# Kernel tuning notes

Hardware: AMD Instinct MI355X
Metric: run time of the kernel (lower is better)

The kernel has to match this reference:

```python
import jax, jax.numpy as jnp
import numpy as np

N_NODES = 50000
N_EDGES = 800000
IN_DIM = 128
HID = 128
OUT_DIM = 128
N_LAYERS = 6
NUM_GRAPHS = 128


def setup_inputs() -> dict:
    key = jax.random.key(0)
    ks = jax.random.split(key, 16)
    s = 0.05
    inp = {
        "x": jax.random.normal(ks[0], (N_NODES, IN_DIM), jnp.float32),
        "edge_index": jax.random.randint(ks[1], (2, N_EDGES), 0, N_NODES, jnp.int64 if jax.config.jax_enable_x64 else jnp.int32).astype(jnp.int32),
        "batch": jnp.sort(jax.random.randint(ks[2], (N_NODES,), 0, NUM_GRAPHS).astype(jnp.int32)),
        # pre linear
        "pre_w": jax.random.normal(ks[3], (IN_DIM, HID), jnp.float32) * s,
        "pre_b": jnp.zeros((HID,), jnp.float32),
        # GIN mlp per layer: Linear(H,H) -> ReLU -> Linear(H,H)
        "conv_w1": jax.random.normal(ks[4], (N_LAYERS, HID, HID), jnp.float32) * s,
        "conv_b1": jnp.zeros((N_LAYERS, HID), jnp.float32),
        "conv_w2": jax.random.normal(ks[5], (N_LAYERS, HID, HID), jnp.float32) * s,
        "conv_b2": jnp.zeros((N_LAYERS, HID), jnp.float32),
        # post MLP: Linear(7H, H) -> ReLU -> Linear(H, out)
        "post_w1": jax.random.normal(ks[6], (HID * (N_LAYERS + 1), HID), jnp.float32) * s,
        "post_b1": jnp.zeros((HID,), jnp.float32),
        "post_w2": jax.random.normal(ks[7], (HID, OUT_DIM), jnp.float32) * s,
        "post_b2": jnp.zeros((OUT_DIM,), jnp.float32),
    }
    return inp


def reference(x, edge_index, batch, pre_w, pre_b, conv_w1, conv_b1, conv_w2, conv_b2,
              post_w1, post_b1, post_w2, post_b2):
    src, dst = edge_index[0], edge_index[1]
    # pre linear
    h = x @ pre_w + pre_b  # [N, H]
    emb_list = [h]
    xres = h
    for i in range(N_LAYERS):
        # GINConv (eps=0): agg_j x_j over in-edges, then (1+eps)*x + agg -> MLP
        msg = h[src]  # [E, H] gather
        agg = jax.ops.segment_sum(msg, dst, num_segments=N_NODES)  # scatter-add
        z = h + agg
        z = jax.nn.relu(z @ conv_w1[i] + conv_b1[i]) @ conv_w2[i] + conv_b2[i]
        if i & 1:
            z = z + xres
            xres = z
        h = jax.nn.relu(z)
        emb_list.append(h)
    emb = jnp.concatenate(emb_list, axis=1)  # [N, (L+1)*H]
    # global add pool over graphs
    pooled = jax.ops.segment_sum(emb, batch, num_segments=NUM_GRAPHS)  # [G, (L+1)*H]
    out = jax.nn.relu(pooled @ post_w1 + post_b1) @ post_w2 + post_b2  # [G, OUT]
    return out
```

## Files before the change

kernel.cpp:

```cpp
#include <hip/hip_runtime.h>
#include <hip/hip_bf16.h>

#define HID 128

using bf16x8 = __attribute__((ext_vector_type(8))) short;
using f32x4  = __attribute__((ext_vector_type(4))) float;

__device__ inline float bf2f(unsigned int u16) {
    union { float f; unsigned int i; } v; v.i = u16 << 16; return v.f;
}
__device__ inline unsigned short f2bf(float f) {
    __hip_bfloat16 h = __float2bfloat16(f);
    return *reinterpret_cast<unsigned short*>(&h);
}


__global__ void zero_i32(int* __restrict__ p, int n) {
    int i = blockIdx.x * blockDim.x + threadIdx.x;
    if (i < n) p[i] = 0;
}

__global__ void count_deg(const int* __restrict__ dst, int* __restrict__ deg, int E) {
    int e = blockIdx.x * blockDim.x + threadIdx.x;
    if (e < E) atomicAdd(&deg[dst[e]], 1);
}

__global__ __launch_bounds__(256) void block_sums(const int* __restrict__ deg,
                                                  int* __restrict__ bsum, int n) {
    __shared__ int red[256];
    int t = threadIdx.x;
    int i = blockIdx.x * 256 + t;
    red[t] = (i < n) ? deg[i] : 0;
    __syncthreads();
    for (int off = 128; off > 0; off >>= 1) {
        if (t < off) red[t] += red[t + off];
        __syncthreads();
    }
    if (t == 0) bsum[blockIdx.x] = red[0];
}

__global__ __launch_bounds__(1024) void scan_bsums(const int* __restrict__ bsum,
                                                   int* __restrict__ bstart, int nb) {
    __shared__ int s[1024];
    int t = threadIdx.x;
    s[t] = (t < nb) ? bsum[t] : 0;
    __syncthreads();
    for (int off = 1; off < 1024; off <<= 1) {
        int v = (t >= off) ? s[t - off] : 0;
        __syncthreads();
        s[t] += v;
        __syncthreads();
    }
    if (t < nb) bstart[t] = (t == 0) ? 0 : s[t - 1];
}

__global__ __launch_bounds__(256) void scan_within(const int* __restrict__ deg,
                                                   const int* __restrict__ bstart,
                                                   int* __restrict__ row_ptr,
                                                   int* __restrict__ pos, int n) {
    __shared__ int s[256];
    int b = blockIdx.x, t = threadIdx.x;
    int i = b * 256 + t;
    int v = (i < n) ? deg[i] : 0;
    s[t] = v;
    __syncthreads();
    for (int off = 1; off < 256; off <<= 1) {
        int u = (t >= off) ? s[t - off] : 0;
        __syncthreads();
        s[t] += u;
        __syncthreads();
    }
    if (i < n) {
        int excl = bstart[b] + s[t] - v;
        row_ptr[i] = excl;
        pos[i] = excl;
        if (i == n - 1) row_ptr[n] = bstart[b] + s[t];
    }
}

__global__ void fill_csr(const int* __restrict__ src, const int* __restrict__ dst,
                         int* __restrict__ pos, int* __restrict__ csr_src, int E) {
    int e = blockIdx.x * blockDim.x + threadIdx.x;
    if (e < E) {
        int p = atomicAdd(&pos[dst[e]], 1);
        csr_src[p] = src[e];
    }
}

__global__ void graph_starts(const int* __restrict__ batch, int* __restrict__ gstart,
                             int n, int G) {
    int g = blockIdx.x * blockDim.x + threadIdx.x;
    if (g > G) return;
    int lo = 0, hi = n;
    while (lo < hi) { int m = (lo + hi) >> 1; if (batch[m] < g) lo = m + 1; else hi = m; }
    gstart[g] = lo;
}


__global__ void f32_to_bf16_vec(const float* __restrict__ in,
                                unsigned short* __restrict__ out, int n8) {
    int i = blockIdx.x * blockDim.x + threadIdx.x;
    if (i >= n8) return;
    const float4* in4 = (const float4*)in;
    float4 a = in4[i * 2], b = in4[i * 2 + 1];
    uint4 o;
    o.x = f2bf(a.x) | ((unsigned)f2bf(a.y) << 16);
    o.y = f2bf(a.z) | ((unsigned)f2bf(a.w) << 16);
    o.z = f2bf(b.x) | ((unsigned)f2bf(b.y) << 16);
    o.w = f2bf(b.z) | ((unsigned)f2bf(b.w) << 16);
    ((uint4*)out)[i] = o;
}

__global__ void transpose_kc(const float* __restrict__ W, unsigned short* __restrict__ Wt,
                             int K, int C, int total) {
    int tid = blockIdx.x * blockDim.x + threadIdx.x;
    if (tid >= total) return;
    int kc = K * C;
    int mat = tid / kc;
    int rem = tid - mat * kc;
    int c = rem / K;
    int k = rem - c * K;
    Wt[tid] = f2bf(W[(size_t)mat * kc + (size_t)k * C + c]);
}

__global__ __launch_bounds__(256) void agg_kernel(const unsigned short* __restrict__ emb,
                                                  int slice_u4, int row_u4,
                                                  const int* __restrict__ row_ptr,
                                                  const int* __restrict__ csr_src,
                                                  unsigned short* __restrict__ z, int N) {
    int node = blockIdx.x * 16 + (threadIdx.x >> 4);
    int lane = threadIdx.x & 15;
    if (node >= N) return;
    const uint4* h4 = (const uint4*)emb;
    uint4 u = h4[(size_t)node * row_u4 + slice_u4 + lane];
    float s0 = bf2f(u.x & 0xffff), s1 = bf2f(u.x >> 16);
    float s2 = bf2f(u.y & 0xffff), s3 = bf2f(u.y >> 16);
    float s4 = bf2f(u.z & 0xffff), s5 = bf2f(u.z >> 16);
    float s6 = bf2f(u.w & 0xffff), s7 = bf2f(u.w >> 16);
    int e0 = row_ptr[node], e1 = row_ptr[node + 1];
    int e = e0;
    for (; e + 3 < e1; e += 4) {
        int sa = csr_src[e], sb = csr_src[e + 1], sc = csr_src[e + 2], sd = csr_src[e + 3];
        uint4 va = h4[(size_t)sa * row_u4 + slice_u4 + lane];
        uint4 vb = h4[(size_t)sb * row_u4 + slice_u4 + lane];
        uint4 vc = h4[(size_t)sc * row_u4 + slice_u4 + lane];
        uint4 vd = h4[(size_t)sd * row_u4 + slice_u4 + lane];
        s0 += bf2f(va.x & 0xffff); s1 += bf2f(va.x >> 16);
        s2 += bf2f(va.y & 0xffff); s3 += bf2f(va.y >> 16);
        s4 += bf2f(va.z & 0xffff); s5 += bf2f(va.z >> 16);
        s6 += bf2f(va.w & 0xffff); s7 += bf2f(va.w >> 16);
        s0 += bf2f(vb.x & 0xffff); s1 += bf2f(vb.x >> 16);
        s2 += bf2f(vb.y & 0xffff); s3 += bf2f(vb.y >> 16);
        s4 += bf2f(vb.z & 0xffff); s5 += bf2f(vb.z >> 16);
        s6 += bf2f(vb.w & 0xffff); s7 += bf2f(vb.w >> 16);
        s0 += bf2f(vc.x & 0xffff); s1 += bf2f(vc.x >> 16);
        s2 += bf2f(vc.y & 0xffff); s3 += bf2f(vc.y >> 16);
        s4 += bf2f(vc.z & 0xffff); s5 += bf2f(vc.z >> 16);
        s6 += bf2f(vc.w & 0xffff); s7 += bf2f(vc.w >> 16);
        s0 += bf2f(vd.x & 0xffff); s1 += bf2f(vd.x >> 16);
        s2 += bf2f(vd.y & 0xffff); s3 += bf2f(vd.y >> 16);
        s4 += bf2f(vd.z & 0xffff); s5 += bf2f(vd.z >> 16);
        s6 += bf2f(vd.w & 0xffff); s7 += bf2f(vd.w >> 16);
    }
    for (; e < e1; e++) {
        uint4 va = h4[(size_t)csr_src[e] * row_u4 + slice_u4 + lane];
        s0 += bf2f(va.x & 0xffff); s1 += bf2f(va.x >> 16);
        s2 += bf2f(va.y & 0xffff); s3 += bf2f(va.y >> 16);
        s4 += bf2f(va.z & 0xffff); s5 += bf2f(va.z >> 16);
        s6 += bf2f(va.w & 0xffff); s7 += bf2f(va.w >> 16);
    }
    uint4 o;
    o.x = f2bf(s0) | ((unsigned)f2bf(s1) << 16);
    o.y = f2bf(s2) | ((unsigned)f2bf(s3) << 16);
    o.z = f2bf(s4) | ((unsigned)f2bf(s5) << 16);
    o.w = f2bf(s6) | ((unsigned)f2bf(s7) << 16);
    ((uint4*)z)[(size_t)node * 16 + lane] = o;
}

template <bool ODD>
__global__ __launch_bounds__(128) void fused_gemm12(const unsigned short* __restrict__ z,
                                                    const unsigned short* __restrict__ Wt1,
                                                    const float* __restrict__ b1,
                                                    const unsigned short* __restrict__ Wt2,
                                                    const float* __restrict__ b2,
                                                    unsigned short* __restrict__ xres,
                                                    unsigned short* __restrict__ h_out,
                                                    int out_stride, int N) {
    __shared__ __align__(16) char lds[16 * 256];
    int t = threadIdx.x;
    int wave = t >> 6, lane = t & 63, l15 = lane & 15, l4 = lane >> 4;
    int rowbase = blockIdx.x * 16;
    int colbase = wave * 64;

    f32x4 acc[4];
#pragma unroll
    for (int ct = 0; ct < 4; ct++) acc[ct] = (f32x4){0.f, 0.f, 0.f, 0.f};

    int r0 = min(rowbase + l15, N - 1);
#pragma unroll
    for (int kk = 0; kk < 4; kk++) {
        int k0 = kk * 32 + l4 * 8;
        bf16x8 a0 = *(const bf16x8*)&z[(size_t)r0 * HID + k0];
#pragma unroll
        for (int ct = 0; ct < 4; ct++) {
            bf16x8 b = *(const bf16x8*)&Wt1[(size_t)(colbase + ct * 16 + l15) * HID + k0];
            acc[ct] = __builtin_amdgcn_mfma_f32_16x16x32_bf16(a0, b, acc[ct], 0, 0, 0);
        }
    }

#pragma unroll
    for (int ct = 0; ct < 4; ct++) {
        int col = colbase + ct * 16 + l15;
        float bc = b1[col];
#pragma unroll
        for (int j = 0; j < 4; j++) {
            int r = l4 * 4 + j;
            float v = fmaxf(acc[ct][j] + bc, 0.f);
            *(unsigned short*)(lds + r * 256 + ((col * 2) ^ ((r & 7) << 4))) = f2bf(v);
        }
    }
    __syncthreads();

#pragma unroll
    for (int ct = 0; ct < 4; ct++) acc[ct] = (f32x4){0.f, 0.f, 0.f, 0.f};
#pragma unroll
    for (int kk = 0; kk < 4; kk++) {
        int k0 = kk * 32 + l4 * 8;
        bf16x8 a0 = *(const bf16x8*)(lds + l15 * 256 + ((k0 * 2) ^ ((l15 & 7) << 4)));
#pragma unroll
        for (int ct = 0; ct < 4; ct++) {
            bf16x8 b = *(const bf16x8*)&Wt2[(size_t)(colbase + ct * 16 + l15) * HID + k0];
            acc[ct] = __builtin_amdgcn_mfma_f32_16x16x32_bf16(a0, b, acc[ct], 0, 0, 0);
        }
    }

#pragma unroll
    for (int ct = 0; ct < 4; ct++) {
        int col = colbase + ct * 16 + l15;
        float bc = b2[col];
#pragma unroll
        for (int j = 0; j < 4; j++) {
            int r = l4 * 4 + j;
            int rg = rowbase + r;
            if (rg < N) {
                float v = acc[ct][j] + bc;
                if (ODD) {
                    v += bf2f(xres[(size_t)rg * HID + col]);
                    xres[(size_t)rg * HID + col] = f2bf(v);
                }
                h_out[(size_t)rg * out_stride + col] = f2bf(fmaxf(v, 0.f));
            }
        }
    }
}

__global__ __launch_bounds__(256) void linear_pre(const unsigned short* __restrict__ in,
                                                  const unsigned short* __restrict__ Wt,
                                                  const float* __restrict__ bias,
                                                  unsigned short* __restrict__ out,
                                                  int out_stride,
                                                  unsigned short* __restrict__ pre_out, int M) {
    int tid = threadIdx.x;
    int wave = tid >> 6, lane = tid & 63;
    int l15 = lane & 15, l4 = lane >> 4;
    int rowbase = blockIdx.x * 64 + wave * 16;
    f32x4 acc[8];
#pragma unroll
    for (int ct = 0; ct < 8; ct++) acc[ct] = (f32x4){0.f, 0.f, 0.f, 0.f};
    int r0 = min(rowbase + l15, M - 1);
#pragma unroll
    for (int kk = 0; kk < 4; kk++) {
        int k0 = kk * 32 + l4 * 8;
        bf16x8 a0 = *(const bf16x8*)&in[(size_t)r0 * HID + k0];
#pragma unroll
        for (int ct = 0; ct < 8; ct++) {
            bf16x8 b = *(const bf16x8*)&Wt[(size_t)(ct * 16 + l15) * HID + k0];
            acc[ct] = __builtin_amdgcn_mfma_f32_16x16x32_bf16(a0, b, acc[ct], 0, 0, 0);
        }
    }
#pragma unroll
    for (int ct = 0; ct < 8; ct++) {
        int col = ct * 16 + l15;
        float bc = bias[col];
#pragma unroll
        for (int j = 0; j < 4; j++) {
            int r = rowbase + l4 * 4 + j;
            if (r < M) {
                float v = acc[ct][j] + bc;
                unsigned short bv = f2bf(v);
                pre_out[(size_t)r * HID + col] = bv;
                out[(size_t)r * out_stride + col] = bv;
            }
        }
    }
}

__global__ __launch_bounds__(128) void pool_all(const unsigned short* __restrict__ emb,
                                                const int* __restrict__ gstart,
                                                float* __restrict__ part, int EMB) {
    int g = blockIdx.x >> 3, sub = blockIdx.x & 7;
    int t = threadIdx.x;
    if (t >= 112) return;
    const uint4* e4 = (const uint4*)emb;
    int row_u4 = EMB / 8;
    int n0 = gstart[g], n1 = gstart[g + 1];
    float s[8] = {0.f, 0.f, 0.f, 0.f, 0.f, 0.f, 0.f, 0.f};
    for (int n = n0 + sub; n < n1; n += 8) {
        uint4 v = e4[(size_t)n * row_u4 + t];
        s[0] += bf2f(v.x & 0xffff); s[1] += bf2f(v.x >> 16);
        s[2] += bf2f(v.y & 0xffff); s[3] += bf2f(v.y >> 16);
        s[4] += bf2f(v.z & 0xffff); s[5] += bf2f(v.z >> 16);
        s[6] += bf2f(v.w & 0xffff); s[7] += bf2f(v.w >> 16);
    }
    float4* p4 = (float4*)&part[(size_t)blockIdx.x * EMB + t * 8];
    p4[0] = (float4){s[0], s[1], s[2], s[3]};
    p4[1] = (float4){s[4], s[5], s[6], s[7]};
}

__global__ __launch_bounds__(128) void pool_fin(const float* __restrict__ part,
                                                unsigned short* __restrict__ pooled,
                                                int EMB) {
    int idx = blockIdx.x * 128 + threadIdx.x;
    int g = idx / EMB, c = idx - g * EMB;
    float s = 0.f;
#pragma unroll
    for (int sub = 0; sub < 8; sub++)
        s += part[(size_t)(g * 8 + sub) * EMB + c];
    pooled[idx] = f2bf(s);
}

__global__ __launch_bounds__(256) void post_mfma(const unsigned short* __restrict__ pooled,
                                                 const unsigned short* __restrict__ w1t,
                                                 const float* __restrict__ b1,
                                                 const unsigned short* __restrict__ w2t,
                                                 const float* __restrict__ b2,
                                                 float* __restrict__ out, int EMB) {
    __shared__ __align__(16) char lds[128 * 256];
    int t = threadIdx.x;
    int wave = t >> 6, lane = t & 63, l15 = lane & 15, l4 = lane >> 4;
    int wrow = wave * 32;
    f32x4 acc[2][8];
#pragma unroll
    for (int rt = 0; rt < 2; rt++)
#pragma unroll
        for (int ct = 0; ct < 8; ct++) acc[rt][ct] = (f32x4){0.f, 0.f, 0.f, 0.f};
    int r0 = wrow + l15, r1 = r0 + 16;
#pragma unroll 4
    for (int kk = 0; kk < EMB / 32; kk++) {
        int k0 = kk * 32 + l4 * 8;
        bf16x8 a0 = *(const bf16x8*)&pooled[(size_t)r0 * EMB + k0];
        bf16x8 a1 = *(const bf16x8*)&pooled[(size_t)r1 * EMB + k0];
#pragma unroll
        for (int ct = 0; ct < 8; ct++) {
            bf16x8 b = *(const bf16x8*)&w1t[(size_t)(ct * 16 + l15) * EMB + k0];
            acc[0][ct] = __builtin_amdgcn_mfma_f32_16x16x32_bf16(a0, b, acc[0][ct], 0, 0, 0);
            acc[1][ct] = __builtin_amdgcn_mfma_f32_16x16x32_bf16(a1, b, acc[1][ct], 0, 0, 0);
        }
    }
#pragma unroll
    for (int ct = 0; ct < 8; ct++) {
        int col = ct * 16 + l15;
        float bc = b1[col];
#pragma unroll
        for (int rt = 0; rt < 2; rt++)
#pragma unroll
            for (int j = 0; j < 4; j++) {
                int r = wrow + rt * 16 + l4 * 4 + j;
                float v = fmaxf(acc[rt][ct][j] + bc, 0.f);
                *(unsigned short*)(lds + r * 256 + ((col * 2) ^ ((r & 7) << 4))) = f2bf(v);
            }
    }
    __syncthreads();
#pragma unroll
    for (int rt = 0; rt < 2; rt++)
#pragma unroll
        for (int ct = 0; ct < 8; ct++) acc[rt][ct] = (f32x4){0.f, 0.f, 0.f, 0.f};
#pragma unroll
    for (int kk = 0; kk < 4; kk++) {
        int k0 = kk * 32 + l4 * 8;
        bf16x8 a0 = *(const bf16x8*)(lds + r0 * 256 + ((k0 * 2) ^ ((r0 & 7) << 4)));
        bf16x8 a1 = *(const bf16x8*)(lds + r1 * 256 + ((k0 * 2) ^ ((r1 & 7) << 4)));
#pragma unroll
        for (int ct = 0; ct < 8; ct++) {
            bf16x8 b = *(const bf16x8*)&w2t[(size_t)(ct * 16 + l15) * HID + k0];
            acc[0][ct] = __builtin_amdgcn_mfma_f32_16x16x32_bf16(a0, b, acc[0][ct], 0, 0, 0);
            acc[1][ct] = __builtin_amdgcn_mfma_f32_16x16x32_bf16(a1, b, acc[1][ct], 0, 0, 0);
        }
    }
#pragma unroll
    for (int ct = 0; ct < 8; ct++) {
        int col = ct * 16 + l15;
        float bc = b2[col];
#pragma unroll
        for (int rt = 0; rt < 2; rt++)
#pragma unroll
            for (int j = 0; j < 4; j++) {
                int r = wrow + rt * 16 + l4 * 4 + j;
                out[(size_t)r * HID + col] = acc[rt][ct][j] + bc;
            }
    }
}


extern "C" void kernel_launch(void* const* d_in, const int* in_sizes, int n_in,
                              void* d_out, int out_size, void* d_ws, size_t ws_size,
                              hipStream_t stream) {
    const float* x       = (const float*)d_in[0];
    const int* edge_index= (const int*)d_in[1];
    const int* batch     = (const int*)d_in[2];
    const float* pre_w   = (const float*)d_in[3];
    const float* pre_b   = (const float*)d_in[4];
    const float* conv_w1 = (const float*)d_in[5];
    const float* conv_b1 = (const float*)d_in[6];
    const float* conv_w2 = (const float*)d_in[7];
    const float* conv_b2 = (const float*)d_in[8];
    const float* post_w1 = (const float*)d_in[9];
    const float* post_b1 = (const float*)d_in[10];
    const float* post_w2 = (const float*)d_in[11];
    const float* post_b2 = (const float*)d_in[12];
    float* outp = (float*)d_out;

    int N = in_sizes[0] / HID;
    int E = in_sizes[1] / 2;
    int L = in_sizes[5] / (HID * HID);
    int G = out_size / HID;
    int EMB = (L + 1) * HID;

    const int* src = edge_index;
    const int* dst = edge_index + E;

    char* w = (char*)d_ws;
    auto alloc = [&](size_t bytes) -> char* {
        char* p = w;
        w += (bytes + 255) & ~(size_t)255;
        return p;
    };
    unsigned short* emb   = (unsigned short*)alloc((size_t)N * EMB * 2);
    unsigned short* z_bf  = (unsigned short*)alloc((size_t)N * HID * 2);
    unsigned short* xres  = (unsigned short*)alloc((size_t)N * HID * 2);
    float* part   = (float*)alloc((size_t)G * 8 * EMB * 4);
    unsigned short* pooled = (unsigned short*)alloc((size_t)G * EMB * 2);
    unsigned short* Wt_pre = (unsigned short*)alloc((size_t)HID * HID * 2);
    unsigned short* Wt_c1  = (unsigned short*)alloc((size_t)L * HID * HID * 2);
    unsigned short* Wt_c2  = (unsigned short*)alloc((size_t)L * HID * HID * 2);
    unsigned short* w1t    = (unsigned short*)alloc((size_t)EMB * HID * 2);
    unsigned short* w2t    = (unsigned short*)alloc((size_t)HID * HID * 2);
    int* deg      = (int*)alloc((size_t)(N + 1) * 4);
    int* row_ptr  = (int*)alloc((size_t)(N + 1) * 4);
    int* pos      = (int*)alloc((size_t)(N + 1) * 4);
    int* bsum     = (int*)alloc((size_t)1024 * 4);
    int* bstart   = (int*)alloc((size_t)1024 * 4);
    int* csr_src  = (int*)alloc((size_t)E * 4);
    int* gstart   = (int*)alloc((size_t)(G + 1) * 4);
    (void)ws_size; (void)n_in;

    int eb = (E + 255) / 256;
    int nb = (N + 255) / 256;

    zero_i32<<<nb, 256, 0, stream>>>(deg, N);
    count_deg<<<eb, 256, 0, stream>>>(dst, deg, E);
    block_sums<<<nb, 256, 0, stream>>>(deg, bsum, N);
    scan_bsums<<<1, 1024, 0, stream>>>(bsum, bstart, nb);
    scan_within<<<nb, 256, 0, stream>>>(deg, bstart, row_ptr, pos, N);
    fill_csr<<<eb, 256, 0, stream>>>(src, dst, pos, csr_src, E);
    graph_starts<<<1, 256, 0, stream>>>(batch, gstart, N, G);

    f32_to_bf16_vec<<<(N * HID / 8 + 255) / 256, 256, 0, stream>>>(x, z_bf, N * HID / 8);
    transpose_kc<<<(HID * HID + 255) / 256, 256, 0, stream>>>(pre_w, Wt_pre, HID, HID, HID * HID);
    transpose_kc<<<(L * HID * HID + 255) / 256, 256, 0, stream>>>(conv_w1, Wt_c1, HID, HID, L * HID * HID);
    transpose_kc<<<(L * HID * HID + 255) / 256, 256, 0, stream>>>(conv_w2, Wt_c2, HID, HID, L * HID * HID);
    transpose_kc<<<(EMB * HID + 255) / 256, 256, 0, stream>>>(post_w1, w1t, EMB, HID, EMB * HID);
    transpose_kc<<<(HID * HID + 255) / 256, 256, 0, stream>>>(post_w2, w2t, HID, HID, HID * HID);

    int gb64 = (N + 63) / 64;
    int gb16 = (N + 15) / 16;

    linear_pre<<<gb64, 256, 0, stream>>>(z_bf, Wt_pre, pre_b, emb, EMB, xres, N);

    for (int i = 0; i < L; i++) {
        agg_kernel<<<gb16, 256, 0, stream>>>(emb, i * 16, EMB / 8, row_ptr, csr_src, z_bf, N);
        unsigned short* slice_out = emb + (size_t)(i + 1) * HID;
        if (i & 1) {
            fused_gemm12<true><<<gb16, 128, 0, stream>>>(
                z_bf, Wt_c1 + (size_t)i * HID * HID, conv_b1 + i * HID,
                Wt_c2 + (size_t)i * HID * HID, conv_b2 + i * HID, xres, slice_out, EMB, N);
        } else {
            fused_gemm12<false><<<gb16, 128, 0, stream>>>(
                z_bf, Wt_c1 + (size_t)i * HID * HID, conv_b1 + i * HID,
                Wt_c2 + (size_t)i * HID * HID, conv_b2 + i * HID, xres, slice_out, EMB, N);
        }
    }

    pool_all<<<G * 8, 128, 0, stream>>>(emb, gstart, part, EMB);
    pool_fin<<<(G * EMB) / 128, 128, 0, stream>>>(part, pooled, EMB);
    post_mfma<<<1, 256, 0, stream>>>(pooled, w1t, post_b1, w2t, post_b2, outp, EMB);
}
```

Before: 586.4 us.

## Fuse neighbor aggregation into the per-layer GIN MLP kernel via LDS

The separate aggregation kernel is folded into the fused two-GEMM layer kernel. Each 128-thread block gathers and sums neighbor rows for its 16 nodes, with 8 threads per node each handling two 16-byte chunks, and writes the result into a swizzled LDS tile that feeds the first MFMA GEMM directly. This removes a kernel launch per layer and the global write/read round trip of the z buffer. In exchange the gather now runs with fewer threads per block and per node and a shallower unroll, so there is less memory-level parallelism for the latency-bound gather.

```diff
diff --git a/kernel.cpp b/kernel.cpp
--- a/kernel.cpp
+++ b/kernel.cpp
@@ -123,84 +123,109 @@
     Wt[tid] = f2bf(W[(size_t)mat * kc + (size_t)k * C + c]);
 }
 
-__global__ __launch_bounds__(256) void agg_kernel(const unsigned short* __restrict__ emb,
-                                                  int slice_u4, int row_u4,
-                                                  const int* __restrict__ row_ptr,
-                                                  const int* __restrict__ csr_src,
-                                                  unsigned short* __restrict__ z, int N) {
-    int node = blockIdx.x * 16 + (threadIdx.x >> 4);
-    int lane = threadIdx.x & 15;
-    if (node >= N) return;
-    const uint4* h4 = (const uint4*)emb;
-    uint4 u = h4[(size_t)node * row_u4 + slice_u4 + lane];
-    float s0 = bf2f(u.x & 0xffff), s1 = bf2f(u.x >> 16);
-    float s2 = bf2f(u.y & 0xffff), s3 = bf2f(u.y >> 16);
-    float s4 = bf2f(u.z & 0xffff), s5 = bf2f(u.z >> 16);
-    float s6 = bf2f(u.w & 0xffff), s7 = bf2f(u.w >> 16);
-    int e0 = row_ptr[node], e1 = row_ptr[node + 1];
-    int e = e0;
-    for (; e + 3 < e1; e += 4) {
-        int sa = csr_src[e], sb = csr_src[e + 1], sc = csr_src[e + 2], sd = csr_src[e + 3];
-        uint4 va = h4[(size_t)sa * row_u4 + slice_u4 + lane];
-        uint4 vb = h4[(size_t)sb * row_u4 + slice_u4 + lane];
-        uint4 vc = h4[(size_t)sc * row_u4 + slice_u4 + lane];
-        uint4 vd = h4[(size_t)sd * row_u4 + slice_u4 + lane];
-        s0 += bf2f(va.x & 0xffff); s1 += bf2f(va.x >> 16);
-        s2 += bf2f(va.y & 0xffff); s3 += bf2f(va.y >> 16);
-        s4 += bf2f(va.z & 0xffff); s5 += bf2f(va.z >> 16);
-        s6 += bf2f(va.w & 0xffff); s7 += bf2f(va.w >> 16);
-        s0 += bf2f(vb.x & 0xffff); s1 += bf2f(vb.x >> 16);
-        s2 += bf2f(vb.y & 0xffff); s3 += bf2f(vb.y >> 16);
-        s4 += bf2f(vb.z & 0xffff); s5 += bf2f(vb.z >> 16);
-        s6 += bf2f(vb.w & 0xffff); s7 += bf2f(vb.w >> 16);
-        s0 += bf2f(vc.x & 0xffff); s1 += bf2f(vc.x >> 16);
-        s2 += bf2f(vc.y & 0xffff); s3 += bf2f(vc.y >> 16);
-        s4 += bf2f(vc.z & 0xffff); s5 += bf2f(vc.z >> 16);
-        s6 += bf2f(vc.w & 0xffff); s7 += bf2f(vc.w >> 16);
-        s0 += bf2f(vd.x & 0xffff); s1 += bf2f(vd.x >> 16);
-        s2 += bf2f(vd.y & 0xffff); s3 += bf2f(vd.y >> 16);
-        s4 += bf2f(vd.z & 0xffff); s5 += bf2f(vd.z >> 16);
-        s6 += bf2f(vd.w & 0xffff); s7 += bf2f(vd.w >> 16);
-    }
-    for (; e < e1; e++) {
-        uint4 va = h4[(size_t)csr_src[e] * row_u4 + slice_u4 + lane];
-        s0 += bf2f(va.x & 0xffff); s1 += bf2f(va.x >> 16);
-        s2 += bf2f(va.y & 0xffff); s3 += bf2f(va.y >> 16);
-        s4 += bf2f(va.z & 0xffff); s5 += bf2f(va.z >> 16);
-        s6 += bf2f(va.w & 0xffff); s7 += bf2f(va.w >> 16);
-    }
-    uint4 o;
-    o.x = f2bf(s0) | ((unsigned)f2bf(s1) << 16);
-    o.y = f2bf(s2) | ((unsigned)f2bf(s3) << 16);
-    o.z = f2bf(s4) | ((unsigned)f2bf(s5) << 16);
-    o.w = f2bf(s6) | ((unsigned)f2bf(s7) << 16);
-    ((uint4*)z)[(size_t)node * 16 + lane] = o;
-}
-
 template <bool ODD>
-__global__ __launch_bounds__(128) void fused_gemm12(const unsigned short* __restrict__ z,
-                                                    const unsigned short* __restrict__ Wt1,
-                                                    const float* __restrict__ b1,
-                                                    const unsigned short* __restrict__ Wt2,
-                                                    const float* __restrict__ b2,
-                                                    unsigned short* __restrict__ xres,
-                                                    unsigned short* __restrict__ h_out,
-                                                    int out_stride, int N) {
-    __shared__ __align__(16) char lds[16 * 256];
+__global__ __launch_bounds__(128) void fused_layer(const unsigned short* __restrict__ emb,
+                                                   int slice_u4, int row_u4,
+                                                   const int* __restrict__ row_ptr,
+                                                   const int* __restrict__ csr_src,
+                                                   const unsigned short* __restrict__ Wt1,
+                                                   const float* __restrict__ b1,
+                                                   const unsigned short* __restrict__ Wt2,
+                                                   const float* __restrict__ b2,
+                                                   unsigned short* __restrict__ xres,
+                                                   unsigned short* __restrict__ h_out,
+                                                   int out_stride, int N) {
+    __shared__ __align__(16) char zt[16 * 256];
+    __shared__ __align__(16) char tt[16 * 256];
     int t = threadIdx.x;
+    int rowbase = blockIdx.x * 16;
+
+    {
+        int nl = t >> 3;
+        int lane8 = t & 7;
+        int node = rowbase + nl;
+        const uint4* h4 = (const uint4*)emb;
+        float sa0=0,sa1=0,sa2=0,sa3=0,sa4=0,sa5=0,sa6=0,sa7=0;
+        float sb0=0,sb1=0,sb2=0,sb3=0,sb4=0,sb5=0,sb6=0,sb7=0;
+        if (node < N) {
+            size_t base = (size_t)node * row_u4 + slice_u4;
+            uint4 u0 = h4[base + lane8];
+            uint4 u1 = h4[base + lane8 + 8];
+            sa0 = bf2f(u0.x & 0xffff); sa1 = bf2f(u0.x >> 16);
+            sa2 = bf2f(u0.y & 0xffff); sa3 = bf2f(u0.y >> 16);
+            sa4 = bf2f(u0.z & 0xffff); sa5 = bf2f(u0.z >> 16);
+            sa6 = bf2f(u0.w & 0xffff); sa7 = bf2f(u0.w >> 16);
+            sb0 = bf2f(u1.x & 0xffff); sb1 = bf2f(u1.x >> 16);
+            sb2 = bf2f(u1.y & 0xffff); sb3 = bf2f(u1.y >> 16);
+            sb4 = bf2f(u1.z & 0xffff); sb5 = bf2f(u1.z >> 16);
+            sb6 = bf2f(u1.w & 0xffff); sb7 = bf2f(u1.w >> 16);
+            int e0 = row_ptr[node], e1 = row_ptr[node + 1];
+            int e = e0;
+            for (; e + 1 < e1; e += 2) {
+                int n0 = csr_src[e], n1 = csr_src[e + 1];
+                size_t p0 = (size_t)n0 * row_u4 + slice_u4;
+                size_t p1 = (size_t)n1 * row_u4 + slice_u4;
+                uint4 v0 = h4[p0 + lane8];
+                uint4 v1 = h4[p0 + lane8 + 8];
+                uint4 w0 = h4[p1 + lane8];
+                uint4 w1 = h4[p1 + lane8 + 8];
+                sa0 += bf2f(v0.x & 0xffff); sa1 += bf2f(v0.x >> 16);
+                sa2 += bf2f(v0.y & 0xffff); sa3 += bf2f(v0.y >> 16);
+                sa4 += bf2f(v0.z & 0xffff); sa5 += bf2f(v0.z >> 16);
+                sa6 += bf2f(v0.w & 0xffff); sa7 += bf2f(v0.w >> 16);
+                sb0 += bf2f(v1.x & 0xffff); sb1 += bf2f(v1.x >> 16);
+                sb2 += bf2f(v1.y & 0xffff); sb3 += bf2f(v1.y >> 16);
+                sb4 += bf2f(v1.z & 0xffff); sb5 += bf2f(v1.z >> 16);
+                sb6 += bf2f(v1.w & 0xffff); sb7 += bf2f(v1.w >> 16);
+                sa0 += bf2f(w0.x & 0xffff); sa1 += bf2f(w0.x >> 16);
+                sa2 += bf2f(w0.y & 0xffff); sa3 += bf2f(w0.y >> 16);
+                sa4 += bf2f(w0.z & 0xffff); sa5 += bf2f(w0.z >> 16);
+                sa6 += bf2f(w0.w & 0xffff); sa7 += bf2f(w0.w >> 16);
+                sb0 += bf2f(w1.x & 0xffff); sb1 += bf2f(w1.x >> 16);
+                sb2 += bf2f(w1.y & 0xffff); sb3 += bf2f(w1.y >> 16);
+                sb4 += bf2f(w1.z & 0xffff); sb5 += bf2f(w1.z >> 16);
+                sb6 += bf2f(w1.w & 0xffff); sb7 += bf2f(w1.w >> 16);
+            }
+            if (e < e1) {
+                size_t p0 = (size_t)csr_src[e] * row_u4 + slice_u4;
+                uint4 v0 = h4[p0 + lane8];
+                uint4 v1 = h4[p0 + lane8 + 8];
+                sa0 += bf2f(v0.x & 0xffff); sa1 += bf2f(v0.x >> 16);
+                sa2 += bf2f(v0.y & 0xffff); sa3 += bf2f(v0.y >> 16);
+                sa4 += bf2f(v0.z & 0xffff); sa5 += bf2f(v0.z >> 16);
+                sa6 += bf2f(v0.w & 0xffff); sa7 += bf2f(v0.w >> 16);
+                sb0 += bf2f(v1.x & 0xffff); sb1 += bf2f(v1.x >> 16);
+                sb2 += bf2f(v1.y & 0xffff); sb3 += bf2f(v1.y >> 16);
+                sb4 += bf2f(v1.z & 0xffff); sb5 += bf2f(v1.z >> 16);
+                sb6 += bf2f(v1.w & 0xffff); sb7 += bf2f(v1.w >> 16);
+            }
+        }
+        uint4 oa, ob;
+        oa.x = f2bf(sa0) | ((unsigned)f2bf(sa1) << 16);
+        oa.y = f2bf(sa2) | ((unsigned)f2bf(sa3) << 16);
+        oa.z = f2bf(sa4) | ((unsigned)f2bf(sa5) << 16);
+        oa.w = f2bf(sa6) | ((unsigned)f2bf(sa7) << 16);
+        ob.x = f2bf(sb0) | ((unsigned)f2bf(sb1) << 16);
+        ob.y = f2bf(sb2) | ((unsigned)f2bf(sb3) << 16);
+        ob.z = f2bf(sb4) | ((unsigned)f2bf(sb5) << 16);
+        ob.w = f2bf(sb6) | ((unsigned)f2bf(sb7) << 16);
+        int swz = (nl & 7) << 4;
+        *(uint4*)(zt + nl * 256 + ((lane8 * 16) ^ swz)) = oa;
+        *(uint4*)(zt + nl * 256 + (((lane8 + 8) * 16) ^ swz)) = ob;
+    }
+    __syncthreads();
+
     int wave = t >> 6, lane = t & 63, l15 = lane & 15, l4 = lane >> 4;
-    int rowbase = blockIdx.x * 16;
     int colbase = wave * 64;
 
     f32x4 acc[4];
 #pragma unroll
     for (int ct = 0; ct < 4; ct++) acc[ct] = (f32x4){0.f, 0.f, 0.f, 0.f};
 
-    int r0 = min(rowbase + l15, N - 1);
 #pragma unroll
     for (int kk = 0; kk < 4; kk++) {
         int k0 = kk * 32 + l4 * 8;
-        bf16x8 a0 = *(const bf16x8*)&z[(size_t)r0 * HID + k0];
+        bf16x8 a0 = *(const bf16x8*)(zt + l15 * 256 + ((k0 * 2) ^ ((l15 & 7) << 4)));
 #pragma unroll
         for (int ct = 0; ct < 4; ct++) {
             bf16x8 b = *(const bf16x8*)&Wt1[(size_t)(colbase + ct * 16 + l15) * HID + k0];
@@ -216,7 +241,7 @@
         for (int j = 0; j < 4; j++) {
             int r = l4 * 4 + j;
             float v = fmaxf(acc[ct][j] + bc, 0.f);
-            *(unsigned short*)(lds + r * 256 + ((col * 2) ^ ((r & 7) << 4))) = f2bf(v);
+            *(unsigned short*)(tt + r * 256 + ((col * 2) ^ ((r & 7) << 4))) = f2bf(v);
         }
     }
     __syncthreads();
@@ -226,7 +251,7 @@
 #pragma unroll
     for (int kk = 0; kk < 4; kk++) {
         int k0 = kk * 32 + l4 * 8;
-        bf16x8 a0 = *(const bf16x8*)(lds + l15 * 256 + ((k0 * 2) ^ ((l15 & 7) << 4)));
+        bf16x8 a0 = *(const bf16x8*)(tt + l15 * 256 + ((k0 * 2) ^ ((l15 & 7) << 4)));
 #pragma unroll
         for (int ct = 0; ct < 4; ct++) {
             bf16x8 b = *(const bf16x8*)&Wt2[(size_t)(colbase + ct * 16 + l15) * HID + k0];
@@ -436,7 +461,7 @@
         return p;
     };
     unsigned short* emb   = (unsigned short*)alloc((size_t)N * EMB * 2);
-    unsigned short* z_bf  = (unsigned short*)alloc((size_t)N * HID * 2);
+    unsigned short* x_bf  = (unsigned short*)alloc((size_t)N * HID * 2);
     unsigned short* xres  = (unsigned short*)alloc((size_t)N * HID * 2);
     float* part   = (float*)alloc((size_t)G * 8 * EMB * 4);
     unsigned short* pooled = (unsigned short*)alloc((size_t)G * EMB * 2);
@@ -465,7 +490,7 @@
     fill_csr<<<eb, 256, 0, stream>>>(src, dst, pos, csr_src, E);
     graph_starts<<<1, 256, 0, stream>>>(batch, gstart, N, G);
 
-    f32_to_bf16_vec<<<(N * HID / 8 + 255) / 256, 256, 0, stream>>>(x, z_bf, N * HID / 8);
+    f32_to_bf16_vec<<<(N * HID / 8 + 255) / 256, 256, 0, stream>>>(x, x_bf, N * HID / 8);
     transpose_kc<<<(HID * HID + 255) / 256, 256, 0, stream>>>(pre_w, Wt_pre, HID, HID, HID * HID);
     transpose_kc<<<(L * HID * HID + 255) / 256, 256, 0, stream>>>(conv_w1, Wt_c1, HID, HID, L * HID * HID);
     transpose_kc<<<(L * HID * HID + 255) / 256, 256, 0, stream>>>(conv_w2, Wt_c2, HID, HID, L * HID * HID);
@@ -475,19 +500,22 @@
     int gb64 = (N + 63) / 64;
     int gb16 = (N + 15) / 16;
 
-    linear_pre<<<gb64, 256, 0, stream>>>(z_bf, Wt_pre, pre_b, emb, EMB, xres, N);
+    linear_pre<<<gb64, 256, 0, stream>>>(x_bf, Wt_pre, pre_b, emb, EMB, xres, N);
 
     for (int i = 0; i < L; i++) {
-        agg_kernel<<<gb16, 256, 0, stream>>>(emb, i * 16, EMB / 8, row_ptr, csr_src, z_bf, N);
         unsigned short* slice_out = emb + (size_t)(i + 1) * HID;
         if (i & 1) {
-            fused_gemm12<true><<<gb16, 128, 0, stream>>>(
-                z_bf, Wt_c1 + (size_t)i * HID * HID, conv_b1 + i * HID,
-                Wt_c2 + (size_t)i * HID * HID, conv_b2 + i * HID, xres, slice_out, EMB, N);
+            fused_layer<true><<<gb16, 128, 0, stream>>>(
+                emb, i * 16, EMB / 8, row_ptr, csr_src,
+                Wt_c1 + (size_t)i * HID * HID, conv_b1 + i * HID,
+                Wt_c2 + (size_t)i * HID * HID, conv_b2 + i * HID,
+                xres, slice_out, EMB, N);
         } else {
-            fused_gemm12<false><<<gb16, 128, 0, stream>>>(
-                z_bf, Wt_c1 + (size_t)i * HID * HID, conv_b1 + i * HID,
-                Wt_c2 + (size_t)i * HID * HID, conv_b2 + i * HID, xres, slice_out, EMB, N);
+            fused_layer<false><<<gb16, 128, 0, stream>>>(
+                emb, i * 16, EMB / 8, row_ptr, csr_src,
+                Wt_c1 + (size_t)i * HID * HID, conv_b1 + i * HID,
+                Wt_c2 + (size_t)i * HID * HID, conv_b2 + i * HID,
+                xres, slice_out, EMB, N);
         }
     }
 
```

Result: no change. 582.0 us (-0.8%).
